# Optimization experiments

Hardware: AMD Instinct MI355X
Metric: run time of the kernel (lower is better)

The kernel has to match this reference:

```python
import jax, jax.numpy as jnp
import numpy as np

NUM_SCENES = 7
SHAPE = [512, 512, 256, 64]  # layer dims: 512->512->256->64
BATCH = 16384


def _xavier(key, shape):
    # nn.init.xavier_normal_ on (s, in, out): fan_in/fan_out from last two dims
    fan_in, fan_out = shape[-2], shape[-1]
    std = np.sqrt(2.0 / (fan_in + fan_out)).astype(np.float32)
    return jax.random.normal(key, shape, dtype=jnp.float32) * std


def setup_inputs() -> dict:
    key = jax.random.key(0)
    ks = jax.random.split(key, 16)
    inp = {
        "x": jax.random.normal(ks[0], (BATCH, SHAPE[0]), dtype=jnp.float32),
        "scene": jax.random.randint(ks[1], (BATCH,), 1, NUM_SCENES + 1, dtype=jnp.int64),
    }
    for i in range(3):
        din, dout = SHAPE[i], SHAPE[i + 1]
        inp[f"W{i}"] = _xavier(ks[2 + 4 * i], (NUM_SCENES, din, dout))
        inp[f"b{i}"] = jnp.zeros((NUM_SCENES, dout), dtype=jnp.float32)
        inp[f"gW{i}"] = _xavier(ks[3 + 4 * i], (1, din, dout))
        inp[f"gb{i}"] = jnp.zeros((1, dout), dtype=jnp.float32)
    return inp


def _star_linear(x, scene0, W, b, gW, gb, relu):
    # W: (S, in, out), gW: (1, in, out). Equivalent to gathering W[scene0]
    # and doing x[:,None,:] @ (w * gW), but computed as a dense GEMM over
    # all scenes followed by a per-sample select (avoids B*in*out gather).
    scaled = W * gW                                   # (S, in, out)
    out_all = jnp.einsum('bi,sio->bso', x, scaled)    # (B, S, out)
    out = jnp.take_along_axis(out_all, scene0[:, None, None], axis=1)[:, 0, :]
    out = out + b[scene0] + gb[0]
    if relu:
        out = jnp.maximum(out, 0.0)
    return out  # dropout is identity at eval


def reference(x, scene, W0, b0, gW0, gb0, W1, b1, gW1, gb1, W2, b2, gW2, gb2):
    scene0 = (scene - 1).astype(jnp.int32)
    h = _star_linear(x, scene0, W0, b0, gW0, gb0, relu=True)
    h = _star_linear(h, scene0, W1, b1, gW1, gb1, relu=True)
    h = _star_linear(h, scene0, W2, b2, gW2, gb2, relu=False)  # drop=True -> no relu
    return h
```

## Files before the change

### kernel.cpp

```cpp
#include <hip/hip_runtime.h>
#include <hip/hip_bf16.h>
#include <stdint.h>


#define BATCH   16384
#define NSCENE  7
#define TM      128
#define NBLK    (BATCH / 256)
#define MT_MAX  (BATCH / TM + NSCENE)
#define PADMAX  (BATCH + NSCENE * TM)

typedef __bf16 bf16x8 __attribute__((ext_vector_type(8)));
typedef float  f32x4  __attribute__((ext_vector_type(4)));

__device__ __forceinline__ ushort f2bf(float f) {
  union { float f; uint32_t u; } v; v.f = f;
  uint32_t r = (v.u + 0x7FFFu + ((v.u >> 16) & 1u)) >> 16;
  return (ushort)r;
}
__device__ __forceinline__ uint32_t pk2(float a, float b) {
  union { __hip_bfloat162 h; uint32_t u; } cv;
  cv.h = __float22bfloat162_rn(make_float2(a, b));
  return cv.u;
}
__device__ __forceinline__ void async16(const void* g, void* lds) {
  __builtin_amdgcn_global_load_lds(
      (const __attribute__((address_space(1))) uint32_t*)g,
      (__attribute__((address_space(3))) uint32_t*)lds, 16, 0, 0);
}

__device__ __forceinline__ void st_tile(const float* __restrict__ W,
                                        const float* __restrict__ gW,
                                        ushort* __restrict__ sT,
                                        int K, int N, int s, int n0, int k0,
                                        int tid) {
  __shared__ float tl[32][33];
  int tx = tid & 31, ty = tid >> 5;
  const float* Wp = W + (size_t)s * K * N;
#pragma unroll
  for (int i = 0; i < 4; i++) {
    int k = k0 + ty + i * 8;
    tl[ty + i * 8][tx] = Wp[(size_t)k * N + n0 + tx] * gW[(size_t)k * N + n0 + tx];
  }
  __syncthreads();
#pragma unroll
  for (int i = 0; i < 4; i++) {
    int n = n0 + ty + i * 8;
    sT[((size_t)s * N + n) * K + k0 + tx] = f2bf(tl[tx][ty + i * 8]);
  }
}

#define NB_W0 (16 * 16 * 7)
#define NB_W1 (8 * 16 * 7)
#define NB_W2 (2 * 8 * 7)
#define NB_BIAS 23
#define NB_CNT NBLK

__global__ __launch_bounds__(256) void prep_k(
    const float* __restrict__ W0, const float* __restrict__ gW0,
    const float* __restrict__ W1, const float* __restrict__ gW1,
    const float* __restrict__ W2, const float* __restrict__ gW2,
    const float* __restrict__ b0, const float* __restrict__ gb0,
    const float* __restrict__ b1, const float* __restrict__ gb1,
    const float* __restrict__ b2, const float* __restrict__ gb2,
    const int* __restrict__ scene,
    ushort* __restrict__ sT0, ushort* __restrict__ sT1, ushort* __restrict__ sT2,
    float* __restrict__ bias0, float* __restrict__ bias1, float* __restrict__ bias2,
    int* __restrict__ bcnt) {
  int bid = blockIdx.x, tid = threadIdx.x;
  if (bid < NB_W0) {
    int l = bid;
    st_tile(W0, gW0, sT0, 512, 512, l / 256, (l % 16) * 32, ((l / 16) % 16) * 32, tid);
  } else if (bid < NB_W0 + NB_W1) {
    int l = bid - NB_W0;
    st_tile(W1, gW1, sT1, 512, 256, l / 128, (l % 8) * 32, ((l / 8) % 16) * 32, tid);
  } else if (bid < NB_W0 + NB_W1 + NB_W2) {
    int l = bid - NB_W0 - NB_W1;
    st_tile(W2, gW2, sT2, 256, 64, l / 16, (l % 2) * 32, ((l / 2) % 8) * 32, tid);
  } else if (bid < NB_W0 + NB_W1 + NB_W2 + NB_BIAS) {
    int t = (bid - NB_W0 - NB_W1 - NB_W2) * 256 + tid;
    if (t < 7 * 512) bias0[t] = b0[t] + gb0[t & 511];
    else if (t < 7 * 512 + 7 * 256) { int i = t - 7 * 512; bias1[i] = b1[i] + gb1[i & 255]; }
    else if (t < 7 * 512 + 7 * 256 + 7 * 64) { int i = t - 7 * 512 - 7 * 256; bias2[i] = b2[i] + gb2[i & 63]; }
  } else {
    __shared__ int l[NSCENE];
    if (tid < NSCENE) l[tid] = 0;
    __syncthreads();
    int blk = bid - NB_W0 - NB_W1 - NB_W2 - NB_BIAS;
    atomicAdd(&l[scene[blk * 256 + tid] - 1], 1);
    __syncthreads();
    if (tid < NSCENE) bcnt[blk * NSCENE + tid] = l[tid];
  }
}

__global__ void plan_k(const int* __restrict__ bcnt, int* __restrict__ meta,
                       int* __restrict__ bbase, int* __restrict__ idxp) {
  __shared__ int tot[NSCENE], pstart[NSCENE], pend[NSCENE];
  int tid = threadIdx.x;
  if (tid < NSCENE) {
    int c = 0;
    for (int b = 0; b < NBLK; b++) c += bcnt[b * NSCENE + tid];
    tot[tid] = c;
  }
  __syncthreads();
  if (tid == 0) {
    int po = 0, t = 0;
    for (int s = 0; s < NSCENE; s++) {
      meta[16 + s] = po;
      int tiles = (tot[s] + TM - 1) / TM;
      pstart[s] = po + tot[s];
      pend[s] = po + tiles * TM;
      for (int j = 0; j < tiles; j++) { meta[32 + t] = s; meta[192 + t] = po + j * TM; t++; }
      po += tiles * TM;
    }
    meta[24] = t;
  }
  __syncthreads();
  if (tid < NSCENE) {
    int run = meta[16 + tid];
    for (int b = 0; b < NBLK; b++) { bbase[b * NSCENE + tid] = run; run += bcnt[b * NSCENE + tid]; }
  }
  for (int s = 0; s < NSCENE; s++)
    for (int i = pstart[s] + tid; i < pend[s]; i += 256) idxp[i] = -1;
}

__global__ void scatter_k(const int* __restrict__ scene,
                          const int* __restrict__ bbase, int* __restrict__ idxp,
                          int* __restrict__ destg) {
  __shared__ int l[NSCENE];
  if (threadIdx.x < NSCENE) l[threadIdx.x] = 0;
  __syncthreads();
  int i = blockIdx.x * 256 + threadIdx.x;
  int s = scene[i] - 1;
  int pos = atomicAdd(&l[s], 1);
  int dest = bbase[blockIdx.x * NSCENE + s] + pos;
  idxp[dest] = i;
  destg[i] = dest;
}

__global__ __launch_bounds__(256) void xc_k(const float* __restrict__ x,
                                            const int* __restrict__ destg,
                                            ushort* __restrict__ xc) {
  int r = blockIdx.x * 8 + (threadIdx.x >> 5);
  int c = (threadIdx.x & 31) * 16;
  int d = destg[r];
  const float4* p = (const float4*)(x + (size_t)r * 512 + c);
  float4 f0 = p[0], f1 = p[1], f2 = p[2], f3 = p[3];
  uint4 v0, v1;
  v0.x = pk2(f0.x, f0.y); v0.y = pk2(f0.z, f0.w);
  v0.z = pk2(f1.x, f1.y); v0.w = pk2(f1.z, f1.w);
  v1.x = pk2(f2.x, f2.y); v1.y = pk2(f2.z, f2.w);
  v1.z = pk2(f3.x, f3.y); v1.w = pk2(f3.z, f3.w);
  uint4* q = (uint4*)(xc + (size_t)d * 512 + c);
  q[0] = v0; q[1] = v1;
}

template<int KDIM, int NDIM, int TN, bool RELU, bool SCATTER_OUT>
__global__ __launch_bounds__(256) void gemm_k(
    const ushort* __restrict__ ain, const ushort* __restrict__ bw,
    const float* __restrict__ bias, const int* __restrict__ meta,
    const int* __restrict__ idxp, ushort* __restrict__ hout,
    float* __restrict__ out) {
  int t = blockIdx.x;
  if (t >= meta[24]) return;
  int sc = meta[32 + t];
  int mrow0 = meta[192 + t];
  int nb = blockIdx.y;

  constexpr int WN = TN / 2;
  constexpr int ACCN = WN / 16;

  __shared__ __align__(16) ushort Abuf[TM * 64];
  __shared__ __align__(16) ushort Bbuf[TN * 64];

  int tid = threadIdx.x;
  int lane = tid & 63, wid = tid >> 6;
  int wm = wid >> 1, wn = wid & 1;

  f32x4 acc[4][ACCN];
#pragma unroll
  for (int mt = 0; mt < 4; mt++)
#pragma unroll
    for (int nt = 0; nt < ACCN; nt++) acc[mt][nt] = (f32x4){0.f, 0.f, 0.f, 0.f};

  const ushort* bwS = bw + ((size_t)sc * NDIM + (size_t)nb * TN) * KDIM;

  for (int kb = 0; kb < KDIM / 64; kb++) {
#pragma unroll
    for (int i = 0; i < 4; i++) {
      int c = tid + i * 256;
      int row = c >> 3, q = c & 7;
      int kg = q ^ (row & 7);
      async16(ain + (size_t)(mrow0 + row) * KDIM + kb * 64 + kg * 8,
              &Abuf[(size_t)(i * 256 + wid * 64) * 8]);
    }
#pragma unroll
    for (int i = 0; i < TN * 8 / 256; i++) {
      int c = tid + i * 256;
      int row = c >> 3, q = c & 7;
      int kg = q ^ (row & 7);
      async16(bwS + (size_t)row * KDIM + kb * 64 + kg * 8,
              &Bbuf[(size_t)(i * 256 + wid * 64) * 8]);
    }
    __syncthreads();
#pragma unroll
    for (int kk = 0; kk < 64; kk += 32) {
      bf16x8 af[4], bfr[ACCN];
      int kc = (kk >> 3) + (lane >> 4);
#pragma unroll
      for (int mt = 0; mt < 4; mt++) {
        int row = wm * 64 + mt * 16 + (lane & 15);
        af[mt] = *(const bf16x8*)(&Abuf[(row * 8 + (kc ^ (row & 7))) * 8]);
      }
#pragma unroll
      for (int nt = 0; nt < ACCN; nt++) {
        int row = wn * WN + nt * 16 + (lane & 15);
        bfr[nt] = *(const bf16x8*)(&Bbuf[(row * 8 + (kc ^ (row & 7))) * 8]);
      }
#pragma unroll
      for (int mt = 0; mt < 4; mt++)
#pragma unroll
        for (int nt = 0; nt < ACCN; nt++)
          acc[mt][nt] = __builtin_amdgcn_mfma_f32_16x16x32_bf16(af[mt], bfr[nt], acc[mt][nt], 0, 0, 0);
    }
    __syncthreads();
  }

  int gidx[4][4];
  if (SCATTER_OUT) {
#pragma unroll
    for (int mt = 0; mt < 4; mt++)
#pragma unroll
      for (int r = 0; r < 4; r++)
        gidx[mt][r] = idxp[mrow0 + wm * 64 + mt * 16 + (lane >> 4) * 4 + r];
  }
#pragma unroll
  for (int mt = 0; mt < 4; mt++) {
    int rl0 = wm * 64 + mt * 16 + (lane >> 4) * 4;
#pragma unroll
    for (int nt = 0; nt < ACCN; nt++) {
      int col = nb * TN + wn * WN + nt * 16 + (lane & 15);
      float bv = bias[sc * NDIM + col];
#pragma unroll
      for (int r = 0; r < 4; r++) {
        float v = acc[mt][nt][r] + bv;
        if (RELU) v = fmaxf(v, 0.f);
        if (SCATTER_OUT) {
          int g = gidx[mt][r];
          if (g >= 0) out[(size_t)g * NDIM + col] = v;
        } else {
          hout[(size_t)(mrow0 + rl0 + r) * NDIM + col] = f2bf(v);
        }
      }
    }
  }
}

extern "C" void kernel_launch(void* const* d_in, const int* in_sizes, int n_in,
                              void* d_out, int out_size, void* d_ws, size_t ws_size,
                              hipStream_t stream) {
  const float* x   = (const float*)d_in[0];
  const int* scene = (const int*)d_in[1];
  const float* W0  = (const float*)d_in[2];
  const float* b0  = (const float*)d_in[3];
  const float* gW0 = (const float*)d_in[4];
  const float* gb0 = (const float*)d_in[5];
  const float* W1  = (const float*)d_in[6];
  const float* b1  = (const float*)d_in[7];
  const float* gW1 = (const float*)d_in[8];
  const float* gb1 = (const float*)d_in[9];
  const float* W2  = (const float*)d_in[10];
  const float* b2  = (const float*)d_in[11];
  const float* gW2 = (const float*)d_in[12];
  const float* gb2 = (const float*)d_in[13];
  float* out = (float*)d_out;

  char* ws = (char*)d_ws;
  size_t off = 0;
  auto alloc = [&](size_t bytes) -> void* {
    void* p = ws + off;
    off = (off + bytes + 255) & ~(size_t)255;
    return p;
  };
  ushort* sT0   = (ushort*)alloc((size_t)7 * 512 * 512 * 2);
  ushort* sT1   = (ushort*)alloc((size_t)7 * 256 * 512 * 2);
  ushort* sT2   = (ushort*)alloc((size_t)7 * 64 * 256 * 2);
  float*  bias0 = (float*)alloc(7 * 512 * 4);
  float*  bias1 = (float*)alloc(7 * 256 * 4);
  float*  bias2 = (float*)alloc(7 * 64 * 4);
  int*    meta  = (int*)alloc(1024 * 4);
  int*    bcnt  = (int*)alloc(NBLK * NSCENE * 4);
  int*    bbase = (int*)alloc(NBLK * NSCENE * 4);
  int*    idxp  = (int*)alloc(PADMAX * 4);
  int*    destg = (int*)alloc(BATCH * 4);
  ushort* xc    = (ushort*)alloc((size_t)PADMAX * 512 * 2);
  ushort* hc1   = (ushort*)alloc((size_t)PADMAX * 512 * 2);
  ushort* hc2   = (ushort*)alloc((size_t)PADMAX * 256 * 2);
  (void)ws_size; (void)n_in; (void)in_sizes; (void)out_size;

  prep_k<<<NB_W0 + NB_W1 + NB_W2 + NB_BIAS + NB_CNT, 256, 0, stream>>>(
      W0, gW0, W1, gW1, W2, gW2, b0, gb0, b1, gb1, b2, gb2, scene,
      sT0, sT1, sT2, bias0, bias1, bias2, bcnt);
  plan_k<<<1, 256, 0, stream>>>(bcnt, meta, bbase, idxp);
  scatter_k<<<NBLK, 256, 0, stream>>>(scene, bbase, idxp, destg);
  xc_k<<<BATCH / 8, 256, 0, stream>>>(x, destg, xc);

  gemm_k<512, 512, 128, true,  false><<<dim3(MT_MAX, 4), 256, 0, stream>>>(
      xc, sT0, bias0, meta, idxp, hc1, nullptr);
  gemm_k<512, 256, 128, true,  false><<<dim3(MT_MAX, 2), 256, 0, stream>>>(
      hc1, sT1, bias1, meta, idxp, hc2, nullptr);
  gemm_k<256, 64,  64,  false, true ><<<dim3(MT_MAX, 1), 256, 0, stream>>>(
      hc2, sT2, bias2, meta, idxp, nullptr, out);
}
```

Before: 170.1 us.

## Fuse scatter with bf16 conversion and fuse layers 1 and 2 into one GEMM kernel

Merges the scatter kernel and the x-to-bf16 gather/convert kernel into one, keeping destinations in shared memory instead of a global destg array. Layers 1 and 2 are fused into a single 512-thread kernel per 128-row tile: the 256-wide hidden activation stays in a swizzled LDS buffer, so the hc2 global round trip and one launch go away. The cost is large LDS use (about 96KB per block), which lowers occupancy. The layer-1 GEMM also drops from two N-blocks per tile to one wide block, which cuts grid parallelism.

```diff
diff --git a/kernel.cpp b/kernel.cpp
--- a/kernel.cpp
+++ b/kernel.cpp
@@ -124,88 +124,87 @@
     for (int i = pstart[s] + tid; i < pend[s]; i += 256) idxp[i] = -1;
 }
 
-__global__ void scatter_k(const int* __restrict__ scene,
-                          const int* __restrict__ bbase, int* __restrict__ idxp,
-                          int* __restrict__ destg) {
+__global__ __launch_bounds__(256) void scatxc_k(const int* __restrict__ scene,
+                                                const int* __restrict__ bbase,
+                                                const float* __restrict__ x,
+                                                int* __restrict__ idxp,
+                                                ushort* __restrict__ xc) {
   __shared__ int l[NSCENE];
-  if (threadIdx.x < NSCENE) l[threadIdx.x] = 0;
-  __syncthreads();
-  int i = blockIdx.x * 256 + threadIdx.x;
+  __shared__ int sdest[256];
+  int tid = threadIdx.x, bid = blockIdx.x;
+  if (tid < NSCENE) l[tid] = 0;
+  __syncthreads();
+  int i = bid * 256 + tid;
   int s = scene[i] - 1;
   int pos = atomicAdd(&l[s], 1);
-  int dest = bbase[blockIdx.x * NSCENE + s] + pos;
+  int dest = bbase[bid * NSCENE + s] + pos;
   idxp[dest] = i;
-  destg[i] = dest;
-}
-
-__global__ __launch_bounds__(256) void xc_k(const float* __restrict__ x,
-                                            const int* __restrict__ destg,
-                                            ushort* __restrict__ xc) {
-  int r = blockIdx.x * 8 + (threadIdx.x >> 5);
-  int c = (threadIdx.x & 31) * 16;
-  int d = destg[r];
-  const float4* p = (const float4*)(x + (size_t)r * 512 + c);
-  float4 f0 = p[0], f1 = p[1], f2 = p[2], f3 = p[3];
-  uint4 v0, v1;
-  v0.x = pk2(f0.x, f0.y); v0.y = pk2(f0.z, f0.w);
-  v0.z = pk2(f1.x, f1.y); v0.w = pk2(f1.z, f1.w);
-  v1.x = pk2(f2.x, f2.y); v1.y = pk2(f2.z, f2.w);
-  v1.z = pk2(f3.x, f3.y); v1.w = pk2(f3.z, f3.w);
-  uint4* q = (uint4*)(xc + (size_t)d * 512 + c);
-  q[0] = v0; q[1] = v1;
-}
-
-template<int KDIM, int NDIM, int TN, bool RELU, bool SCATTER_OUT>
-__global__ __launch_bounds__(256) void gemm_k(
+  sdest[tid] = dest;
+  __syncthreads();
+  int rbase = bid * 256;
+#pragma unroll 4
+  for (int p = 0; p < 32; p++) {
+    int rl = p * 8 + (tid >> 5);
+    int c = (tid & 31) * 16;
+    int d = sdest[rl];
+    const float4* pp = (const float4*)(x + (size_t)(rbase + rl) * 512 + c);
+    float4 f0 = pp[0], f1 = pp[1], f2 = pp[2], f3 = pp[3];
+    uint4 v0, v1;
+    v0.x = pk2(f0.x, f0.y); v0.y = pk2(f0.z, f0.w);
+    v0.z = pk2(f1.x, f1.y); v0.w = pk2(f1.z, f1.w);
+    v1.x = pk2(f2.x, f2.y); v1.y = pk2(f2.z, f2.w);
+    v1.z = pk2(f3.x, f3.y); v1.w = pk2(f3.z, f3.w);
+    uint4* q = (uint4*)(xc + (size_t)d * 512 + c);
+    q[0] = v0; q[1] = v1;
+  }
+}
+
+__global__ __launch_bounds__(256) void gemm0_k(
     const ushort* __restrict__ ain, const ushort* __restrict__ bw,
     const float* __restrict__ bias, const int* __restrict__ meta,
-    const int* __restrict__ idxp, ushort* __restrict__ hout,
-    float* __restrict__ out) {
+    ushort* __restrict__ hout) {
   int t = blockIdx.x;
   if (t >= meta[24]) return;
   int sc = meta[32 + t];
   int mrow0 = meta[192 + t];
   int nb = blockIdx.y;
 
-  constexpr int WN = TN / 2;
-  constexpr int ACCN = WN / 16;
-
   __shared__ __align__(16) ushort Abuf[TM * 64];
-  __shared__ __align__(16) ushort Bbuf[TN * 64];
+  __shared__ __align__(16) ushort Bbuf[TM * 64];
 
   int tid = threadIdx.x;
   int lane = tid & 63, wid = tid >> 6;
   int wm = wid >> 1, wn = wid & 1;
 
-  f32x4 acc[4][ACCN];
+  f32x4 acc[4][4];
 #pragma unroll
   for (int mt = 0; mt < 4; mt++)
 #pragma unroll
-    for (int nt = 0; nt < ACCN; nt++) acc[mt][nt] = (f32x4){0.f, 0.f, 0.f, 0.f};
-
-  const ushort* bwS = bw + ((size_t)sc * NDIM + (size_t)nb * TN) * KDIM;
-
-  for (int kb = 0; kb < KDIM / 64; kb++) {
+    for (int nt = 0; nt < 4; nt++) acc[mt][nt] = (f32x4){0.f, 0.f, 0.f, 0.f};
+
+  const ushort* bwS = bw + ((size_t)sc * 512 + (size_t)nb * 128) * 512;
+
+  for (int kb = 0; kb < 8; kb++) {
 #pragma unroll
     for (int i = 0; i < 4; i++) {
       int c = tid + i * 256;
       int row = c >> 3, q = c & 7;
       int kg = q ^ (row & 7);
-      async16(ain + (size_t)(mrow0 + row) * KDIM + kb * 64 + kg * 8,
+      async16(ain + (size_t)(mrow0 + row) * 512 + kb * 64 + kg * 8,
               &Abuf[(size_t)(i * 256 + wid * 64) * 8]);
     }
 #pragma unroll
-    for (int i = 0; i < TN * 8 / 256; i++) {
+    for (int i = 0; i < 4; i++) {
       int c = tid + i * 256;
       int row = c >> 3, q = c & 7;
       int kg = q ^ (row & 7);
-      async16(bwS + (size_t)row * KDIM + kb * 64 + kg * 8,
+      async16(bwS + (size_t)row * 512 + kb * 64 + kg * 8,
               &Bbuf[(size_t)(i * 256 + wid * 64) * 8]);
     }
     __syncthreads();
 #pragma unroll
     for (int kk = 0; kk < 64; kk += 32) {
-      bf16x8 af[4], bfr[ACCN];
+      bf16x8 af[4], bfr[4];
       int kc = (kk >> 3) + (lane >> 4);
 #pragma unroll
       for (int mt = 0; mt < 4; mt++) {
@@ -213,45 +212,163 @@
         af[mt] = *(const bf16x8*)(&Abuf[(row * 8 + (kc ^ (row & 7))) * 8]);
       }
 #pragma unroll
-      for (int nt = 0; nt < ACCN; nt++) {
-        int row = wn * WN + nt * 16 + (lane & 15);
+      for (int nt = 0; nt < 4; nt++) {
+        int row = wn * 64 + nt * 16 + (lane & 15);
         bfr[nt] = *(const bf16x8*)(&Bbuf[(row * 8 + (kc ^ (row & 7))) * 8]);
       }
 #pragma unroll
       for (int mt = 0; mt < 4; mt++)
 #pragma unroll
-        for (int nt = 0; nt < ACCN; nt++)
+        for (int nt = 0; nt < 4; nt++)
           acc[mt][nt] = __builtin_amdgcn_mfma_f32_16x16x32_bf16(af[mt], bfr[nt], acc[mt][nt], 0, 0, 0);
     }
     __syncthreads();
   }
 
-  int gidx[4][4];
-  if (SCATTER_OUT) {
-#pragma unroll
-    for (int mt = 0; mt < 4; mt++)
-#pragma unroll
-      for (int r = 0; r < 4; r++)
-        gidx[mt][r] = idxp[mrow0 + wm * 64 + mt * 16 + (lane >> 4) * 4 + r];
-  }
 #pragma unroll
   for (int mt = 0; mt < 4; mt++) {
     int rl0 = wm * 64 + mt * 16 + (lane >> 4) * 4;
 #pragma unroll
-    for (int nt = 0; nt < ACCN; nt++) {
-      int col = nb * TN + wn * WN + nt * 16 + (lane & 15);
-      float bv = bias[sc * NDIM + col];
+    for (int nt = 0; nt < 4; nt++) {
+      int col = nb * 128 + wn * 64 + nt * 16 + (lane & 15);
+      float bv = bias[sc * 512 + col];
 #pragma unroll
       for (int r = 0; r < 4; r++) {
-        float v = acc[mt][nt][r] + bv;
-        if (RELU) v = fmaxf(v, 0.f);
-        if (SCATTER_OUT) {
-          int g = gidx[mt][r];
-          if (g >= 0) out[(size_t)g * NDIM + col] = v;
-        } else {
-          hout[(size_t)(mrow0 + rl0 + r) * NDIM + col] = f2bf(v);
-        }
-      }
+        float v = fmaxf(acc[mt][nt][r] + bv, 0.f);
+        hout[(size_t)(mrow0 + rl0 + r) * 512 + col] = f2bf(v);
+      }
+    }
+  }
+}
+
+__global__ __launch_bounds__(512) void gemm12_k(
+    const ushort* __restrict__ hc1, const ushort* __restrict__ sT1,
+    const ushort* __restrict__ sT2, const float* __restrict__ bias1,
+    const float* __restrict__ bias2, const int* __restrict__ meta,
+    const int* __restrict__ idxp, float* __restrict__ out) {
+  int t = blockIdx.x;
+  if (t >= meta[24]) return;
+  int sc = meta[32 + t];
+  int mrow0 = meta[192 + t];
+
+  __shared__ __align__(16) ushort Abuf[128 * 64];
+  __shared__ __align__(16) ushort Bbuf[256 * 64];
+  __shared__ __align__(16) ushort h2[128 * 256];
+
+  int tid = threadIdx.x;
+  int lane = tid & 63, wid = tid >> 6;
+  int wm = wid >> 2, wn = wid & 3;
+
+  f32x4 acc[4][4];
+#pragma unroll
+  for (int mt = 0; mt < 4; mt++)
+#pragma unroll
+    for (int nt = 0; nt < 4; nt++) acc[mt][nt] = (f32x4){0.f, 0.f, 0.f, 0.f};
+
+  const ushort* b1p = sT1 + (size_t)sc * 256 * 512;
+
+  for (int kb = 0; kb < 8; kb++) {
+#pragma unroll
+    for (int i = 0; i < 2; i++) {
+      int c = tid + i * 512;
+      int row = c >> 3, q = c & 7;
+      int kg = q ^ (row & 7);
+      async16(hc1 + (size_t)(mrow0 + row) * 512 + kb * 64 + kg * 8,
+              &Abuf[(size_t)(i * 512 + wid * 64) * 8]);
+    }
+#pragma unroll
+    for (int i = 0; i < 4; i++) {
+      int c = tid + i * 512;
+      int row = c >> 3, q = c & 7;
+      int kg = q ^ (row & 7);
+      async16(b1p + (size_t)row * 512 + kb * 64 + kg * 8,
+              &Bbuf[(size_t)(i * 512 + wid * 64) * 8]);
+    }
+    __syncthreads();
+#pragma unroll
+    for (int kk = 0; kk < 64; kk += 32) {
+      bf16x8 af[4], bfr[4];
+      int kc = (kk >> 3) + (lane >> 4);
+#pragma unroll
+      for (int mt = 0; mt < 4; mt++) {
+        int row = wm * 64 + mt * 16 + (lane & 15);
+        af[mt] = *(const bf16x8*)(&Abuf[(row * 8 + (kc ^ (row & 7))) * 8]);
+      }
+#pragma unroll
+      for (int nt = 0; nt < 4; nt++) {
+        int row = wn * 64 + nt * 16 + (lane & 15);
+        bfr[nt] = *(const bf16x8*)(&Bbuf[(row * 8 + (kc ^ (row & 7))) * 8]);
+      }
+#pragma unroll
+      for (int mt = 0; mt < 4; mt++)
+#pragma unroll
+        for (int nt = 0; nt < 4; nt++)
+          acc[mt][nt] = __builtin_amdgcn_mfma_f32_16x16x32_bf16(af[mt], bfr[nt], acc[mt][nt], 0, 0, 0);
+    }
+    __syncthreads();
+  }
+
+#pragma unroll
+  for (int mt = 0; mt < 4; mt++) {
+#pragma unroll
+    for (int nt = 0; nt < 4; nt++) {
+      int col = wn * 64 + nt * 16 + (lane & 15);
+      float bv = bias1[sc * 256 + col];
+#pragma unroll
+      for (int r = 0; r < 4; r++) {
+        int row = wm * 64 + mt * 16 + (lane >> 4) * 4 + r;
+        float v = fmaxf(acc[mt][nt][r] + bv, 0.f);
+        h2[(row * 32 + ((col >> 3) ^ (row & 7))) * 8 + (col & 7)] = f2bf(v);
+      }
+    }
+  }
+  __syncthreads();
+
+  f32x4 acc2[4];
+#pragma unroll
+  for (int mt = 0; mt < 4; mt++) acc2[mt] = (f32x4){0.f, 0.f, 0.f, 0.f};
+
+  const ushort* b2p = sT2 + (size_t)sc * 64 * 256;
+
+  for (int kb = 0; kb < 4; kb++) {
+    {
+      int c = tid;
+      int row = c >> 3, q = c & 7;
+      int kg = q ^ (row & 7);
+      async16(b2p + (size_t)row * 256 + kb * 64 + kg * 8,
+              &Bbuf[(size_t)(wid * 64) * 8]);
+    }
+    __syncthreads();
+#pragma unroll
+    for (int kk = 0; kk < 64; kk += 32) {
+      bf16x8 af[4], bfr;
+      int kc = (kk >> 3) + (lane >> 4);
+      int kf = kb * 8 + kc;
+#pragma unroll
+      for (int mt = 0; mt < 4; mt++) {
+        int row = wm * 64 + mt * 16 + (lane & 15);
+        af[mt] = *(const bf16x8*)(&h2[(row * 32 + (kf ^ (row & 7))) * 8]);
+      }
+      {
+        int n = wn * 16 + (lane & 15);
+        bfr = *(const bf16x8*)(&Bbuf[(n * 8 + (kc ^ (n & 7))) * 8]);
+      }
+#pragma unroll
+      for (int mt = 0; mt < 4; mt++)
+        acc2[mt] = __builtin_amdgcn_mfma_f32_16x16x32_bf16(af[mt], bfr, acc2[mt], 0, 0, 0);
+    }
+    __syncthreads();
+  }
+
+  int col = wn * 16 + (lane & 15);
+  float bv = bias2[sc * 64 + col];
+#pragma unroll
+  for (int mt = 0; mt < 4; mt++) {
+    int rl0 = wm * 64 + mt * 16 + (lane >> 4) * 4;
+#pragma unroll
+    for (int r = 0; r < 4; r++) {
+      int g = idxp[mrow0 + rl0 + r];
+      if (g >= 0) out[(size_t)g * 64 + col] = acc2[mt][r] + bv;
     }
   }
 }
@@ -292,23 +409,17 @@
   int*    bcnt  = (int*)alloc(NBLK * NSCENE * 4);
   int*    bbase = (int*)alloc(NBLK * NSCENE * 4);
   int*    idxp  = (int*)alloc(PADMAX * 4);
-  int*    destg = (int*)alloc(BATCH * 4);
   ushort* xc    = (ushort*)alloc((size_t)PADMAX * 512 * 2);
   ushort* hc1   = (ushort*)alloc((size_t)PADMAX * 512 * 2);
-  ushort* hc2   = (ushort*)alloc((size_t)PADMAX * 256 * 2);
   (void)ws_size; (void)n_in; (void)in_sizes; (void)out_size;
 
   prep_k<<<NB_W0 + NB_W1 + NB_W2 + NB_BIAS + NB_CNT, 256, 0, stream>>>(
       W0, gW0, W1, gW1, W2, gW2, b0, gb0, b1, gb1, b2, gb2, scene,
       sT0, sT1, sT2, bias0, bias1, bias2, bcnt);
   plan_k<<<1, 256, 0, stream>>>(bcnt, meta, bbase, idxp);
-  scatter_k<<<NBLK, 256, 0, stream>>>(scene, bbase, idxp, destg);
-  xc_k<<<BATCH / 8, 256, 0, stream>>>(x, destg, xc);
-
-  gemm_k<512, 512, 128, true,  false><<<dim3(MT_MAX, 4), 256, 0, stream>>>(
-      xc, sT0, bias0, meta, idxp, hc1, nullptr);
-  gemm_k<512, 256, 128, true,  false><<<dim3(MT_MAX, 2), 256, 0, stream>>>(
-      hc1, sT1, bias1, meta, idxp, hc2, nullptr);
-  gemm_k<256, 64,  64,  false, true ><<<dim3(MT_MAX, 1), 256, 0, stream>>>(
-      hc2, sT2, bias2, meta, idxp, nullptr, out);
-}
+  scatxc_k<<<NBLK, 256, 0, stream>>>(scene, bbase, x, idxp, xc);
+
+  gemm0_k<<<dim3(MT_MAX, 4), 256, 0, stream>>>(xc, sT0, bias0, meta, hc1);
+  gemm12_k<<<dim3(MT_MAX), 512, 0, stream>>>(hc1, sT1, sT2, bias1, bias2,
+                                             meta, idxp, out);
+}
```

Result: slower. 187.0 us (+9.9%).
